# Performance work log

Measured on AMD Instinct MI355X. Metric: run time of the kernel, lower is better.

## Reference

```python
import jax, jax.numpy as jnp
import numpy as np

N_NODES = 100000
N_EDGES = 640000
HIDDEN = 128


def setup_inputs() -> dict:
    key = jax.random.key(0)
    k1, k2, k3, k4 = jax.random.split(key, 4)
    node_emb = jax.random.normal(k1, (N_NODES, HIDDEN), dtype=jnp.float32)
    edge_index = jax.random.randint(k2, (2, N_EDGES), 0, N_NODES, dtype=jnp.int64)
    # edge head params: Linear(2H -> H), Linear(H -> 2)
    s1 = 1.0 / np.sqrt(2 * HIDDEN)
    s2 = 1.0 / np.sqrt(HIDDEN)
    W1 = jax.random.uniform(k3, (2 * HIDDEN, HIDDEN), jnp.float32, -s1, s1)
    b1 = jnp.zeros((HIDDEN,), jnp.float32)
    W2 = jax.random.uniform(k4, (HIDDEN, 2), jnp.float32, -s2, s2)
    b2 = jnp.zeros((2,), jnp.float32)
    return {"node_emb": node_emb, "edge_index": edge_index,
            "W1": W1, "b1": b1, "W2": W2, "b2": b2}


def reference(node_emb, edge_index, W1, b1, W2, b2):
    # gather src/dst node embeddings by edge_index (irregular gather)
    src, dst = edge_index[0], edge_index[1]
    edge_emb = jnp.concatenate([node_emb[src], node_emb[dst]], axis=-1)  # [E, 2H]
    # edge head: Linear -> ReLU -> (Dropout = identity in eval) -> Linear
    h = jax.nn.relu(edge_emb @ W1 + b1)  # [E, H]
    flow_pred = h @ W2 + b2              # [E, 2]
    return flow_pred
```

## Files before the change

kernel.cpp:

```cpp
#include <hip/hip_runtime.h>

typedef __attribute__((ext_vector_type(8))) short short8;
typedef __attribute__((ext_vector_type(4))) short short4v;
typedef __attribute__((ext_vector_type(4))) float floatx4;

static __device__ __forceinline__ unsigned short f2bf(float f) {
    union { float f; unsigned int u; } v; v.f = f;
    unsigned int u = v.u;
    return (unsigned short)((u + 0x7FFFu + ((u >> 16) & 1u)) >> 16);
}
static __device__ __forceinline__ float bf2f(short x) {
    return __uint_as_float(((unsigned int)(unsigned short)x) << 16);
}

__global__ void cvt_wt_kernel(const float* __restrict__ w1,
                              unsigned short* __restrict__ wt) {
    __shared__ unsigned short sT[32 * 130];
    const int b = blockIdx.x;
    const int kg0 = b * 32;
    const int h = (kg0 >= 128) ? 1 : 0;
    const int kk0 = kg0 & 127;
    const int tid = threadIdx.x;
#pragma unroll
    for (int i = 0; i < 16; i++) {
        int idx = tid + i * 256;
        int k = idx >> 7, n = idx & 127;
        sT[k * 130 + n] = f2bf(w1[(kg0 + k) * 128 + n]);
    }
    __syncthreads();
#pragma unroll
    for (int i = 0; i < 16; i++) {
        int idx = tid + i * 256;
        int n = idx >> 5, k = idx & 31;
        wt[(h * 128 + n) * 128 + kk0 + k] = sT[k * 130 + n];
    }
}

__global__ __launch_bounds__(256) void node_gemm_kernel(
    float* xy,
    const unsigned short* __restrict__ wt,
    const float* __restrict__ b1, int N)
{
    __shared__ unsigned short sW[256 * 128];

    const int tid = threadIdx.x;
    const int lane = tid & 63, wave = tid >> 6;
    const int l15 = lane & 15, lq = lane >> 4;

#pragma unroll
    for (int i = 0; i < 16; i++) {
        int u = tid + i * 256;
        int r = u >> 4, s = u & 15;
        *(short8*)&sW[r * 128 + ((s ^ r) & 15) * 8] =
            *(const short8*)&wt[r * 128 + s * 8];
    }
    __syncthreads();

    const int n0 = blockIdx.x * 64 + wave * 16;
    const int nr = n0 + l15;
    const int nc = (nr < N) ? nr : (N - 1);
    const float* xrow = xy + (size_t)nc * 128;

    floatx4 acc[16];
#pragma unroll
    for (int mt = 0; mt < 16; mt++) acc[mt] = (floatx4){0.f, 0.f, 0.f, 0.f};

#pragma unroll
    for (int ks = 0; ks < 4; ks++) {
        const float4 xa = *(const float4*)(xrow + ks * 32 + lq * 8);
        const float4 xb = *(const float4*)(xrow + ks * 32 + lq * 8 + 4);
        short8 bf;
        bf[0] = (short)f2bf(xa.x); bf[1] = (short)f2bf(xa.y);
        bf[2] = (short)f2bf(xa.z); bf[3] = (short)f2bf(xa.w);
        bf[4] = (short)f2bf(xb.x); bf[5] = (short)f2bf(xb.y);
        bf[6] = (short)f2bf(xb.z); bf[7] = (short)f2bf(xb.w);
#pragma unroll
        for (int mt = 0; mt < 16; mt++) {
            const short8 af = *(const short8*)
                &sW[(mt * 16 + l15) * 128 + (((ks * 4 + lq) ^ l15) & 15) * 8];
            acc[mt] = __builtin_amdgcn_mfma_f32_16x16x32_bf16(af, bf, acc[mt], 0, 0, 0);
        }
    }

    if (nr < N) {
        unsigned short* yrow = (unsigned short*)xy + (size_t)nr * 256;
#pragma unroll
        for (int mt = 0; mt < 16; mt++) {
            const int oc = mt * 16 + lq * 4;
            float4 bb = (mt < 8) ? *(const float4*)&b1[oc]
                                 : (float4){0.f, 0.f, 0.f, 0.f};
            short4v pk;
            pk[0] = (short)f2bf(acc[mt][0] + bb.x);
            pk[1] = (short)f2bf(acc[mt][1] + bb.y);
            pk[2] = (short)f2bf(acc[mt][2] + bb.z);
            pk[3] = (short)f2bf(acc[mt][3] + bb.w);
            *(short4v*)(yrow + oc) = pk;
        }
    }
}

__global__ __launch_bounds__(256) void edge_kernel(
    const unsigned short* __restrict__ Y,
    const int* __restrict__ eidx,
    const float* __restrict__ w2,
    const float* __restrict__ b2,
    float* __restrict__ out,
    int E, int n_nodes)
{
    const int tid = threadIdx.x;
    const int lane = tid & 63, wave = tid >> 6;
    const int r = lane >> 4, cl = lane & 15;

    float w20[8], w21[8];
#pragma unroll
    for (int q = 0; q < 4; q++) {
        const float4 f = *(const float4*)&w2[cl * 16 + q * 4];
        w20[q * 2]     = f.x; w21[q * 2]     = f.y;
        w20[q * 2 + 1] = f.z; w21[q * 2 + 1] = f.w;
    }
    const float bb0 = b2[0], bb1 = b2[1];

    const long eb = (long)blockIdx.x * 256 + wave * 64;
    const char* Yb = (const char*)Y;

    int sg[4], dg[4];
#pragma unroll
    for (int g = 0; g < 4; g++) {
        long e = eb + g * 4 + r; if (e >= E) e = E - 1;
        int s = eidx[e], d = eidx[(long)E + e];
        sg[g] = (s < 0) ? 0 : (s >= n_nodes ? n_nodes - 1 : s);
        dg[g] = (d < 0) ? 0 : (d >= n_nodes ? n_nodes - 1 : d);
    }

    for (int ch = 0; ch < 4; ch++) {
        const long e0 = eb + ch * 16;
        short8 v1[4], v2[4];
#pragma unroll
        for (int g = 0; g < 4; g++) {
            v1[g] = *(const short8*)(Yb + (size_t)sg[g] * 512 + cl * 16);
            v2[g] = *(const short8*)(Yb + (size_t)dg[g] * 512 + 256 + cl * 16);
        }
        if (ch < 3) {
#pragma unroll
            for (int g = 0; g < 4; g++) {
                long e = e0 + 16 + g * 4 + r; if (e >= E) e = E - 1;
                int s = eidx[e], d = eidx[(long)E + e];
                sg[g] = (s < 0) ? 0 : (s >= n_nodes ? n_nodes - 1 : s);
                dg[g] = (d < 0) ? 0 : (d >= n_nodes ? n_nodes - 1 : d);
            }
        }
#pragma unroll
        for (int g = 0; g < 4; g++) {
            float p0 = 0.f, p1 = 0.f;
#pragma unroll
            for (int j = 0; j < 8; j++) {
                float f = bf2f(v1[g][j]) + bf2f(v2[g][j]);
                f = fmaxf(f, 0.f);
                p0 = fmaf(f, w20[j], p0);
                p1 = fmaf(f, w21[j], p1);
            }
#pragma unroll
            for (int m = 1; m < 16; m <<= 1) {
                p0 += __shfl_xor(p0, m, 64);
                p1 += __shfl_xor(p1, m, 64);
            }
            if (cl == 0) {
                const long e = e0 + g * 4 + r;
                if (e < E) {
                    float2 o; o.x = p0 + bb0; o.y = p1 + bb1;
                    *(float2*)&out[e * 2] = o;
                }
            }
        }
    }
}

extern "C" void kernel_launch(void* const* d_in, const int* in_sizes, int n_in,
                              void* d_out, int out_size, void* d_ws, size_t ws_size,
                              hipStream_t stream) {
    float*       xy   = (float*)d_in[0];
    const int*   eidx = (const int*)d_in[1];
    const float* W1   = (const float*)d_in[2];
    const float* b1   = (const float*)d_in[3];
    const float* W2   = (const float*)d_in[4];
    const float* b2   = (const float*)d_in[5];
    float* out = (float*)d_out;

    const int n_node_elems = in_sizes[0];
    const int N = n_node_elems / 128;
    const int E = in_sizes[1] / 2;

    unsigned short* wt = (unsigned short*)d_ws;

    cvt_wt_kernel<<<8, 256, 0, stream>>>(W1, wt);

    const int nblk1 = (N + 63) / 64;
    node_gemm_kernel<<<nblk1, 256, 0, stream>>>(xy, wt, b1, N);

    const int nblk2 = (E + 255) / 256;
    edge_kernel<<<nblk2, 256, 0, stream>>>((const unsigned short*)xy, eidx,
                                           W2, b2, out, E, N);
}
```

Before: 166.8 us.

## Double-buffer edge gathers, widen node GEMM blocks, hoist input loads, nontemporal I/O

The edge kernel now keeps two chunks of gathered Y rows in flight, prefetching indices two chunks ahead and issuing the next gather after compute, to hide gather latency. The node GEMM uses 512-thread blocks covering 128 nodes, which halves the per-block shared-memory weight staging relative to nodes processed. It also loads 64 floats of each input row up front. Index loads and output stores use nontemporal hints. The extra buffers raise register pressure in the edge kernel, and the launch bounds (512, 4) may force register spilling in the GEMM.

Measured after the change: 163.5 us, median of 2. Within noise of the previous version (-2.0%).

```diff
diff --git a/kernel.cpp b/kernel.cpp
--- a/kernel.cpp
+++ b/kernel.cpp
@@ -3,6 +3,7 @@
 typedef __attribute__((ext_vector_type(8))) short short8;
 typedef __attribute__((ext_vector_type(4))) short short4v;
 typedef __attribute__((ext_vector_type(4))) float floatx4;
+typedef __attribute__((ext_vector_type(2))) float floatx2;
 
 static __device__ __forceinline__ unsigned short f2bf(float f) {
     union { float f; unsigned int u; } v; v.f = f;
@@ -36,7 +37,7 @@
     }
 }
 
-__global__ __launch_bounds__(256) void node_gemm_kernel(
+__global__ __launch_bounds__(512, 4) void node_gemm_kernel(
     float* xy,
     const unsigned short* __restrict__ wt,
     const float* __restrict__ b1, int N)
@@ -48,16 +49,15 @@
     const int l15 = lane & 15, lq = lane >> 4;
 
 #pragma unroll
-    for (int i = 0; i < 16; i++) {
-        int u = tid + i * 256;
+    for (int i = 0; i < 8; i++) {
+        int u = tid + i * 512;
         int r = u >> 4, s = u & 15;
         *(short8*)&sW[r * 128 + ((s ^ r) & 15) * 8] =
             *(const short8*)&wt[r * 128 + s * 8];
     }
     __syncthreads();
 
-    const int n0 = blockIdx.x * 64 + wave * 16;
-    const int nr = n0 + l15;
+    const int nr = blockIdx.x * 128 + wave * 16 + l15;
     const int nc = (nr < N) ? nr : (N - 1);
     const float* xrow = xy + (size_t)nc * 128;
 
@@ -66,19 +66,34 @@
     for (int mt = 0; mt < 16; mt++) acc[mt] = (floatx4){0.f, 0.f, 0.f, 0.f};
 
 #pragma unroll
-    for (int ks = 0; ks < 4; ks++) {
-        const float4 xa = *(const float4*)(xrow + ks * 32 + lq * 8);
-        const float4 xb = *(const float4*)(xrow + ks * 32 + lq * 8 + 4);
-        short8 bf;
-        bf[0] = (short)f2bf(xa.x); bf[1] = (short)f2bf(xa.y);
-        bf[2] = (short)f2bf(xa.z); bf[3] = (short)f2bf(xa.w);
-        bf[4] = (short)f2bf(xb.x); bf[5] = (short)f2bf(xb.y);
-        bf[6] = (short)f2bf(xb.z); bf[7] = (short)f2bf(xb.w);
-#pragma unroll
-        for (int mt = 0; mt < 16; mt++) {
-            const short8 af = *(const short8*)
-                &sW[(mt * 16 + l15) * 128 + (((ks * 4 + lq) ^ l15) & 15) * 8];
-            acc[mt] = __builtin_amdgcn_mfma_f32_16x16x32_bf16(af, bf, acc[mt], 0, 0, 0);
+    for (int kh = 0; kh < 2; kh++) {
+        float4 xf[4];
+#pragma unroll
+        for (int q = 0; q < 4; q++)
+            xf[q] = *(const float4*)(xrow + kh * 64 + (q >> 1) * 32 + lq * 8
+                                     + (q & 1) * 4);
+        short8 bf[2];
+#pragma unroll
+        for (int t = 0; t < 2; t++) {
+            bf[t][0] = (short)f2bf(xf[2 * t].x);
+            bf[t][1] = (short)f2bf(xf[2 * t].y);
+            bf[t][2] = (short)f2bf(xf[2 * t].z);
+            bf[t][3] = (short)f2bf(xf[2 * t].w);
+            bf[t][4] = (short)f2bf(xf[2 * t + 1].x);
+            bf[t][5] = (short)f2bf(xf[2 * t + 1].y);
+            bf[t][6] = (short)f2bf(xf[2 * t + 1].z);
+            bf[t][7] = (short)f2bf(xf[2 * t + 1].w);
+        }
+#pragma unroll
+        for (int t = 0; t < 2; t++) {
+            const int ks = kh * 2 + t;
+#pragma unroll
+            for (int mt = 0; mt < 16; mt++) {
+                const short8 af = *(const short8*)
+                    &sW[(mt * 16 + l15) * 128 + (((ks * 4 + lq) ^ l15) & 15) * 8];
+                acc[mt] = __builtin_amdgcn_mfma_f32_16x16x32_bf16(af, bf[t],
+                                                                  acc[mt], 0, 0, 0);
+            }
         }
     }
 
@@ -124,37 +139,37 @@
     const char* Yb = (const char*)Y;
 
     int sg[4], dg[4];
-#pragma unroll
-    for (int g = 0; g < 4; g++) {
-        long e = eb + g * 4 + r; if (e >= E) e = E - 1;
-        int s = eidx[e], d = eidx[(long)E + e];
-        sg[g] = (s < 0) ? 0 : (s >= n_nodes ? n_nodes - 1 : s);
-        dg[g] = (d < 0) ? 0 : (d >= n_nodes ? n_nodes - 1 : d);
-    }
+    short8 buf[2][2][4];
+
+#define LOAD_IDX(CH)                                                        \
+    _Pragma("unroll")                                                       \
+    for (int g = 0; g < 4; g++) {                                           \
+        long e = eb + (CH) * 16 + g * 4 + r; if (e >= E) e = E - 1;         \
+        int s = __builtin_nontemporal_load(&eidx[e]);                       \
+        int d = __builtin_nontemporal_load(&eidx[(long)E + e]);             \
+        sg[g] = (s < 0) ? 0 : (s >= n_nodes ? n_nodes - 1 : s);             \
+        dg[g] = (d < 0) ? 0 : (d >= n_nodes ? n_nodes - 1 : d);             \
+    }
+#define LOAD_Y(P)                                                           \
+    _Pragma("unroll")                                                       \
+    for (int g = 0; g < 4; g++) {                                           \
+        buf[P][0][g] = *(const short8*)(Yb + (size_t)sg[g] * 512 + cl * 16);\
+        buf[P][1][g] = *(const short8*)(Yb + (size_t)dg[g] * 512 + 256      \
+                                        + cl * 16);                         \
+    }
+
+    LOAD_IDX(0); LOAD_Y(0);
+    LOAD_IDX(1); LOAD_Y(1);
 
     for (int ch = 0; ch < 4; ch++) {
-        const long e0 = eb + ch * 16;
-        short8 v1[4], v2[4];
-#pragma unroll
-        for (int g = 0; g < 4; g++) {
-            v1[g] = *(const short8*)(Yb + (size_t)sg[g] * 512 + cl * 16);
-            v2[g] = *(const short8*)(Yb + (size_t)dg[g] * 512 + 256 + cl * 16);
-        }
-        if (ch < 3) {
-#pragma unroll
-            for (int g = 0; g < 4; g++) {
-                long e = e0 + 16 + g * 4 + r; if (e >= E) e = E - 1;
-                int s = eidx[e], d = eidx[(long)E + e];
-                sg[g] = (s < 0) ? 0 : (s >= n_nodes ? n_nodes - 1 : s);
-                dg[g] = (d < 0) ? 0 : (d >= n_nodes ? n_nodes - 1 : d);
-            }
-        }
+        const int p = ch & 1;
+        if (ch < 2) { LOAD_IDX(ch + 2); }
 #pragma unroll
         for (int g = 0; g < 4; g++) {
             float p0 = 0.f, p1 = 0.f;
 #pragma unroll
             for (int j = 0; j < 8; j++) {
-                float f = bf2f(v1[g][j]) + bf2f(v2[g][j]);
+                float f = bf2f(buf[p][0][g][j]) + bf2f(buf[p][1][g][j]);
                 f = fmaxf(f, 0.f);
                 p0 = fmaf(f, w20[j], p0);
                 p1 = fmaf(f, w21[j], p1);
@@ -165,14 +180,18 @@
                 p1 += __shfl_xor(p1, m, 64);
             }
             if (cl == 0) {
-                const long e = e0 + g * 4 + r;
+                const long e = eb + ch * 16 + g * 4 + r;
                 if (e < E) {
-                    float2 o; o.x = p0 + bb0; o.y = p1 + bb1;
-                    *(float2*)&out[e * 2] = o;
+                    floatx2 o;
+                    o.x = p0 + bb0; o.y = p1 + bb1;
+                    __builtin_nontemporal_store(o, (floatx2*)&out[e * 2]);
                 }
             }
         }
-    }
+        if (ch < 2) { LOAD_Y(p); }
+    }
+#undef LOAD_IDX
+#undef LOAD_Y
 }
 
 extern "C" void kernel_launch(void* const* d_in, const int* in_sizes, int n_in,
@@ -194,8 +213,8 @@
 
     cvt_wt_kernel<<<8, 256, 0, stream>>>(W1, wt);
 
-    const int nblk1 = (N + 63) / 64;
-    node_gemm_kernel<<<nblk1, 256, 0, stream>>>(xy, wt, b1, N);
+    const int nblk1 = (N + 127) / 128;
+    node_gemm_kernel<<<nblk1, 512, 0, stream>>>(xy, wt, b1, N);
 
     const int nblk2 = (E + 255) / 256;
     edge_kernel<<<nblk2, 256, 0, stream>>>((const unsigned short*)xy, eidx,
```
